# Kernel tuning notes

Hardware: AMD Instinct MI355X
Metric: run time of the kernel (lower is better)

The kernel has to match this reference:

```python
import jax, jax.numpy as jnp
import numpy as np

ATOM_DIM, HID, N_LAYERS, N_HEADS, PF_DIM = 34, 256, 2, 8, 1024
B, NA, NP = 32, 512, 1024


def setup_inputs() -> dict:
    key = jax.random.key(0)
    ks = iter(jax.random.split(key, 32))
    def rn(shape, s=0.02):
        return jax.random.normal(next(ks), shape, dtype=jnp.float32) * s
    L = N_LAYERS
    z = lambda *s: jnp.zeros(s, jnp.float32)
    return {
        "trg": jax.random.normal(next(ks), (B, NA, ATOM_DIM), dtype=jnp.float32),
        "src": jax.random.normal(next(ks), (B, NP, HID), dtype=jnp.float32),
        "ft_w": rn((HID, ATOM_DIM)), "ft_b": z(HID),
        "ln_g": jnp.ones((L, HID), jnp.float32), "ln_b": z(L, HID),
        "sa_wq": rn((L, HID, HID)), "sa_bq": z(L, HID),
        "sa_wk": rn((L, HID, HID)), "sa_bk": z(L, HID),
        "sa_wv": rn((L, HID, HID)), "sa_bv": z(L, HID),
        "sa_wf": rn((L, HID, HID)), "sa_bf": z(L, HID),
        "ea_wq": rn((L, HID, HID)), "ea_bq": z(L, HID),
        "ea_wk": rn((L, HID, HID)), "ea_bk": z(L, HID),
        "ea_wv": rn((L, HID, HID)), "ea_bv": z(L, HID),
        "ea_wf": rn((L, HID, HID)), "ea_bf": z(L, HID),
        "pf_w1": rn((L, PF_DIM, HID)), "pf_b1": z(L, PF_DIM),
        "pf_w2": rn((L, HID, PF_DIM)), "pf_b2": z(L, HID),
        "fc1_w": rn((256, HID)), "fc1_b": z(256),
        "fc2_w": rn((2, 256)), "fc2_b": z(2),
    }


def _ln(x, g, b, eps=1e-5):
    m = jnp.mean(x, axis=-1, keepdims=True)
    v = jnp.mean(jnp.square(x - m), axis=-1, keepdims=True)
    return (x - m) * jax.lax.rsqrt(v + eps) * g + b


def _attn(xq, xkv, wq, bq, wk, bk, wv, bv, wf, bf):
    b_, lq, h = xq.shape
    d = h // N_HEADS
    q = (xq @ wq.T + bq).reshape(b_, lq, N_HEADS, d).transpose(0, 2, 1, 3)
    k = (xkv @ wk.T + bk).reshape(b_, -1, N_HEADS, d).transpose(0, 2, 1, 3)
    v = (xkv @ wv.T + bv).reshape(b_, -1, N_HEADS, d).transpose(0, 2, 1, 3)
    scale = jnp.sqrt(jnp.float32(d))  # TransformerCPI: sqrt(hid_dim // n_heads)
    a = jax.nn.softmax(jnp.einsum('bhqd,bhkd->bhqk', q, k) / scale, axis=-1)
    o = jnp.einsum('bhqk,bhkd->bhqd', a, v).transpose(0, 2, 1, 3).reshape(b_, lq, h)
    return o @ wf.T + bf


def reference(trg, src, ft_w, ft_b, ln_g, ln_b,
              sa_wq, sa_bq, sa_wk, sa_bk, sa_wv, sa_bv, sa_wf, sa_bf,
              ea_wq, ea_bq, ea_wk, ea_bk, ea_wv, ea_bv, ea_wf, ea_bf,
              pf_w1, pf_b1, pf_w2, pf_b2, fc1_w, fc1_b, fc2_w, fc2_b):
    x = trg @ ft_w.T + ft_b  # [B, NA, HID]
    for l in range(N_LAYERS):
        x = _ln(x + _attn(x, x, sa_wq[l], sa_bq[l], sa_wk[l], sa_bk[l],
                          sa_wv[l], sa_bv[l], sa_wf[l], sa_bf[l]), ln_g[l], ln_b[l])
        x = _ln(x + _attn(x, src, ea_wq[l], ea_bq[l], ea_wk[l], ea_bk[l],
                          ea_wv[l], ea_bv[l], ea_wf[l], ea_bf[l]), ln_g[l], ln_b[l])
        h = jax.nn.relu(x @ pf_w1[l].T + pf_b1[l]) @ pf_w2[l].T + pf_b2[l]
        x = _ln(x + h, ln_g[l], ln_b[l])
    # norm-weighted attention pooling (replaces the nested Python loops)
    w = jax.nn.softmax(jnp.linalg.norm(x, axis=2), axis=1)  # [B, NA]
    pooled = jnp.einsum('bn,bnh->bh', w, x)  # [B, HID]
    return jax.nn.relu(pooled @ fc1_w.T + fc1_b) @ fc2_w.T + fc2_b
```

## Files before the change

kernel.cpp:

```cpp
#include <hip/hip_runtime.h>
#include <hip/hip_bf16.h>
#include <math.h>

#define B_   32
#define NA   512
#define NP   1024
#define HID  256
#define NH   8
#define DH   32
#define PF   1024

typedef short bf16x8 __attribute__((ext_vector_type(8)));
typedef float f32x4  __attribute__((ext_vector_type(4)));
typedef float f32x16 __attribute__((ext_vector_type(16)));
typedef unsigned u32x4 __attribute__((ext_vector_type(4)));

#define ZERO16 {0.f,0.f,0.f,0.f,0.f,0.f,0.f,0.f,0.f,0.f,0.f,0.f,0.f,0.f,0.f,0.f}

static __device__ inline unsigned short f2bf(float f) {
    __hip_bfloat16 h = __float2bfloat16(f);
    unsigned short u;
    __builtin_memcpy(&u, &h, 2);
    return u;
}
static __device__ inline float bf2f(unsigned short u) {
    unsigned x = ((unsigned)u) << 16;
    return __uint_as_float(x);
}
static __device__ inline unsigned cvtpk(float lo, float hi) {
    return (unsigned)f2bf(lo) | ((unsigned)f2bf(hi) << 16);
}
static __device__ inline bf16x8 pack8(float4 a, float4 b) {
    bf16x8 r;
    r[0] = (short)f2bf(a.x); r[1] = (short)f2bf(a.y);
    r[2] = (short)f2bf(a.z); r[3] = (short)f2bf(a.w);
    r[4] = (short)f2bf(b.x); r[5] = (short)f2bf(b.y);
    r[6] = (short)f2bf(b.z); r[7] = (short)f2bf(b.w);
    return r;
}
static __device__ inline void gload16(const unsigned short* g, unsigned short* l) {
    __builtin_amdgcn_global_load_lds(
        (const __attribute__((address_space(1))) void*)g,
        (__attribute__((address_space(3))) void*)l, 16, 0, 0);
}

__global__ __launch_bounds__(256) void ft_kernel(const float* __restrict__ trg,
    const float* __restrict__ w, const float* __restrict__ b,
    float* __restrict__ out, unsigned short* __restrict__ outb)
{
    __shared__ float Ws[256][35];
    int tid = threadIdx.x;
    for (int k = 0; k < 34; ++k) Ws[tid][k] = w[tid*34 + k];
    float bias = b[tid];
    __syncthreads();
    int m0 = blockIdx.x * 32;
    for (int r = 0; r < 32; ++r) {
        int m = m0 + r;
        const float* tr = trg + (size_t)m*34;
        float acc = bias;
        #pragma unroll
        for (int k = 0; k < 34; ++k) acc += tr[k] * Ws[tid][k];
        out [(size_t)m*HID + tid] = acc;
        outb[(size_t)m*HID + tid] = f2bf(acc);
    }
}

__global__ __launch_bounds__(256) void cvt_bf16(const float* __restrict__ in,
    unsigned short* __restrict__ outb, int n8)
{
    int i = blockIdx.x*256 + threadIdx.x;
    int stride = gridDim.x*256;
    for (; i < n8; i += stride) {
        float4 a = *(const float4*)(in + (size_t)i*8);
        float4 b = *(const float4*)(in + (size_t)i*8 + 4);
        *(bf16x8*)(outb + (size_t)i*8) = pack8(a, b);
    }
}

__global__ __launch_bounds__(256) void cvt_w(
    const float* __restrict__ s0, const float* __restrict__ s1,
    const float* __restrict__ s2, const float* __restrict__ s3,
    const float* __restrict__ s4, const float* __restrict__ s5,
    const float* __restrict__ s6, const float* __restrict__ s7,
    const float* __restrict__ s8, const float* __restrict__ s9,
    unsigned short* __restrict__ dst)
{
    const int z = blockIdx.z;
    const float* src;
    switch (z) {
        case 0: src = s0; break; case 1: src = s1; break;
        case 2: src = s2; break; case 3: src = s3; break;
        case 4: src = s4; break; case 5: src = s5; break;
        case 6: src = s6; break; case 7: src = s7; break;
        case 8: src = s8; break; default: src = s9; break;
    }
    const int n8 = (z < 8) ? 16384 : 65536;
    const size_t off = (z < 8) ? (size_t)z*131072 : (1048576u + (size_t)(z-8)*524288);
    unsigned short* o = dst + off;
    int i = blockIdx.x*256 + threadIdx.x;
    const int stride = gridDim.x*256;
    for (; i < n8; i += stride) {
        float4 a = *(const float4*)(src + (size_t)i*8);
        float4 b = *(const float4*)(src + (size_t)i*8 + 4);
        *(bf16x8*)(o + (size_t)i*8) = pack8(a, b);
    }
}

static __device__ inline void gemm_core(const unsigned short* __restrict__ Ab,
    const unsigned short* __restrict__ Wb, const float* __restrict__ bias,
    void* __restrict__ Cv, int M, int N, int K, int mode, int L, float oscale,
    int bx, int by)
{
    __shared__ __attribute__((aligned(16))) unsigned short As[2][128*64];
    __shared__ __attribute__((aligned(16))) unsigned short Ws[2][64*64];
    const int tid = threadIdx.x;
    const int wave = tid >> 6, lane = tid & 63, lq = lane & 15, g = lane >> 4;
    const int wr = wave >> 1, wc = wave & 1;
    const int m0 = by * 128, n0 = bx * 64;

    const int srow = lane >> 3;
    const int scol = ((lane & 7) ^ ((lane >> 3) & 7)) * 8;
    const int cswz = (lq & 7) * 8;

    f32x4 acc[4][2] = {};

    auto STAGE = [&](int kt, int buf) {
        const int k0 = kt * 64;
        #pragma unroll
        for (int c = 0; c < 4; ++c) {
            const int row = wave*32 + c*8;
            gload16(Ab + (size_t)(m0 + row + srow)*K + k0 + scol,
                    &As[buf][row*64]);
        }
        #pragma unroll
        for (int c = 0; c < 2; ++c) {
            const int row = wave*16 + c*8;
            gload16(Wb + (size_t)(n0 + row + srow)*K + k0 + scol,
                    &Ws[buf][row*64]);
        }
    };

    const int nk = K / 64;
    STAGE(0, 0);
    __syncthreads();
    for (int kt = 0; kt < nk; ++kt) {
        const int cur = kt & 1;
        if (kt + 1 < nk) STAGE(kt + 1, cur ^ 1);
        const unsigned short* Ac = &As[cur][0];
        const unsigned short* Wc = &Ws[cur][0];
        #pragma unroll
        for (int ks = 0; ks < 2; ++ks) {
            const int co = (ks*32 + g*8) ^ cswz;
            bf16x8 bf0 = *(const bf16x8*)&Wc[(wc*32 +  0 + lq)*64 + co];
            bf16x8 bf1 = *(const bf16x8*)&Wc[(wc*32 + 16 + lq)*64 + co];
            #pragma unroll
            for (int i = 0; i < 4; ++i) {
                bf16x8 af = *(const bf16x8*)&Ac[(wr*64 + i*16 + lq)*64 + co];
                acc[i][0] = __builtin_amdgcn_mfma_f32_16x16x32_bf16(af, bf0, acc[i][0], 0, 0, 0);
                acc[i][1] = __builtin_amdgcn_mfma_f32_16x16x32_bf16(af, bf1, acc[i][1], 0, 0, 0);
            }
        }
        __syncthreads();
    }

    float bb[2];
    #pragma unroll
    for (int j = 0; j < 2; ++j) bb[j] = bias[n0 + wc*32 + j*16 + lq];

    #pragma unroll
    for (int i = 0; i < 4; ++i) {
        const int mb = m0 + wr*64 + i*16 + 4*g;
        #pragma unroll
        for (int j = 0; j < 2; ++j) {
            const int n = n0 + wc*32 + j*16 + lq;
            f32x4 v = acc[i][j];
            #pragma unroll
            for (int r = 0; r < 4; ++r) v[r] = (v[r] + bb[j]) * oscale;
            if (mode == 1) {
                unsigned short* Cb = (unsigned short*)Cv;
                #pragma unroll
                for (int r = 0; r < 4; ++r) Cb[(size_t)(mb + r)*N + n] = f2bf(v[r]);
            } else if (mode == 3) {
                unsigned short* Cb = (unsigned short*)Cv;
                #pragma unroll
                for (int r = 0; r < 4; ++r) Cb[(size_t)(mb + r)*N + n] = f2bf(fmaxf(v[r], 0.f));
            } else if (mode == 4) {
                unsigned short* Cb = (unsigned short*)Cv;
                const int bI = mb / L, kk = mb % L;
                const int hh = n >> 5, d = n & 31;
                const int t2 = kk >> 5, dc = d >> 4, hi2 = (d >> 3) & 1;
                unsigned short* base = Cb
                    + ((size_t)(((bI*NH + hh)*(L >> 5) + t2)*2 + dc))*512
                    + ((kk & 31) + 32*hi2)*8 + (d & 7);
                base[0]  = f2bf(v[0]); base[8]  = f2bf(v[1]);
                base[16] = f2bf(v[2]); base[24] = f2bf(v[3]);
            } else {
                unsigned short* Cb = (unsigned short*)Cv;
                const int bI = mb / L, kk = mb % L;
                const int hh = n >> 5, d = n & 31;
                const int t = kk >> 6, oct = (kk >> 3) & 7;
                const int c = oct >> 1, hiV = oct & 1;
                ushort4 pk;
                pk.x = f2bf(v[0]); pk.y = f2bf(v[1]); pk.z = f2bf(v[2]); pk.w = f2bf(v[3]);
                *(ushort4*)(Cb
                    + ((size_t)(((bI*NH + hh)*(L >> 6) + t)*4 + c))*512
                    + (d + 32*hiV)*8 + (kk & 7)) = pk;
            }
        }
    }
}

static __device__ inline void xcd_swz(int d, int nx, int nxy, int& bx, int& by)
{
    const int w = (d & 7) * (nxy >> 3) + (d >> 3);
    bx = w % nx; by = w / nx;
}

__global__ __launch_bounds__(256) void gemm_mfma(const unsigned short* __restrict__ A,
    const unsigned short* __restrict__ W, const float* __restrict__ bias,
    void* __restrict__ C, int M, int N, int K, int mode, int L)
{
    int bx, by;
    xcd_swz(blockIdx.y*gridDim.x + blockIdx.x, gridDim.x, gridDim.x*gridDim.y, bx, by);
    gemm_core(A, W, bias, C, M, N, K, mode, L, 1.f, bx, by);
}

__global__ __launch_bounds__(256) void qkv_mfma(const unsigned short* __restrict__ Aq,
    const unsigned short* __restrict__ Akv,
    const unsigned short* __restrict__ Wq, const float* __restrict__ bq,
    const unsigned short* __restrict__ Wk, const float* __restrict__ bk,
    const unsigned short* __restrict__ Wv, const float* __restrict__ bv,
    void* __restrict__ qo, void* __restrict__ ko, void* __restrict__ vo,
    int Mq, int Mkv, int L)
{
    const int z = blockIdx.z;
    const unsigned short* A = (z == 0) ? Aq : Akv;
    const unsigned short* W = (z == 0) ? Wq : ((z == 1) ? Wk : Wv);
    const float* bb = (z == 0) ? bq : ((z == 1) ? bk : bv);
    void* C = (z == 0) ? qo : ((z == 1) ? ko : vo);
    const int M = (z == 0) ? Mq : Mkv;
    const int mode = (z == 0) ? 1 : ((z == 1) ? 4 : 5);
    const float sc = (z == 0) ? 0.25504082364238727f : 1.f;
    int bx, by;
    xcd_swz(blockIdx.y*gridDim.x + blockIdx.x, gridDim.x, gridDim.x*gridDim.y, bx, by);
    if (by * 128 >= M) return;
    gemm_core(A, W, bb, C, M, HID, HID, mode, L, sc, bx, by);
}

__global__ __launch_bounds__(512) void gemm_ln(const unsigned short* __restrict__ Ab,
    const unsigned short* __restrict__ Wb, const float* __restrict__ bias,
    const float* __restrict__ lng, const float* __restrict__ lnb,
    float* __restrict__ x, unsigned short* __restrict__ xb,
    float* __restrict__ nrm, int K)
{
    __shared__ __attribute__((aligned(16))) char smem[81920];
    unsigned short* As0 = (unsigned short*)smem;
    unsigned short* Ws0 = (unsigned short*)(smem + 16384);
    float* ys = (float*)smem;
    const int tid = threadIdx.x;
    const int w = tid >> 6, lane = tid & 63, lq = lane & 15, g = lane >> 4;
    const int wc2 = w & 3, wh = w >> 2;
    const int m0 = blockIdx.x * 64;

    const int srow = lane >> 3;
    const int scol = ((lane & 7) ^ srow) * 8;
    const int cswz = (lq & 7) * 8;

    f32x4 acc[4][2] = {};

    auto STAGE = [&](int kt, int buf) {
        const int k0 = kt * 64;
        {   const int row = w * 8;
            gload16(Ab + (size_t)(m0 + row + srow)*K + k0 + scol,
                    As0 + buf*4096 + row*64);
        }
        #pragma unroll
        for (int c = 0; c < 4; ++c) {
            const int row = w*32 + c*8;
            gload16(Wb + (size_t)(row + srow)*K + k0 + scol,
                    Ws0 + buf*16384 + row*64);
        }
    };

    const int nk = K / 64;
    STAGE(0, 0);
    __syncthreads();
    for (int kt = 0; kt < nk; ++kt) {
        const int cur = kt & 1;
        if (kt + 1 < nk) STAGE(kt + 1, cur ^ 1);
        const unsigned short* Ac = As0 + cur*4096;
        const unsigned short* Wc = Ws0 + cur*16384;
        #pragma unroll
        for (int ks = 0; ks < 2; ++ks) {
            const int co = (ks*32 + g*8) ^ cswz;
            bf16x8 bf0 = *(const bf16x8*)&Wc[(wc2*64 + wh*32 +  0 + lq)*64 + co];
            bf16x8 bf1 = *(const bf16x8*)&Wc[(wc2*64 + wh*32 + 16 + lq)*64 + co];
            #pragma unroll
            for (int i = 0; i < 4; ++i) {
                bf16x8 af = *(const bf16x8*)&Ac[(i*16 + lq)*64 + co];
                acc[i][0] = __builtin_amdgcn_mfma_f32_16x16x32_bf16(af, bf0, acc[i][0], 0, 0, 0);
                acc[i][1] = __builtin_amdgcn_mfma_f32_16x16x32_bf16(af, bf1, acc[i][1], 0, 0, 0);
            }
        }
        __syncthreads();
    }

    float bb0 = bias[wc2*64 + wh*32 +  0 + lq];
    float bb1 = bias[wc2*64 + wh*32 + 16 + lq];
    #pragma unroll
    for (int i = 0; i < 4; ++i) {
        const int col0 = wc2*64 + wh*32 + lq;
        #pragma unroll
        for (int r = 0; r < 4; ++r) {
            const int row = i*16 + 4*g + r;
            ys[row*260 + col0]      = acc[i][0][r] + bb0;
            ys[row*260 + col0 + 16] = acc[i][1][r] + bb1;
        }
    }
    __syncthreads();

    float4 gv = *(const float4*)(lng + lane*4);
    float4 bv = *(const float4*)(lnb + lane*4);
    for (int it = 0; it < 8; ++it) {
        const int row = w*8 + it;
        const size_t gbase = (size_t)(m0 + row)*HID + lane*4;
        float4 y = *(float4*)&ys[row*260 + lane*4];
        float4 xv = *(const float4*)(x + gbase);
        y.x += xv.x; y.y += xv.y; y.z += xv.z; y.w += xv.w;
        float s = y.x + y.y + y.z + y.w;
        #pragma unroll
        for (int o = 32; o > 0; o >>= 1) s += __shfl_xor(s, o);
        float mean = s * (1.f/256.f);
        float4 d = {y.x - mean, y.y - mean, y.z - mean, y.w - mean};
        float q2 = d.x*d.x + d.y*d.y + d.z*d.z + d.w*d.w;
        #pragma unroll
        for (int o = 32; o > 0; o >>= 1) q2 += __shfl_xor(q2, o);
        float rs = rsqrtf(q2*(1.f/256.f) + 1e-5f);
        float4 ov;
        ov.x = d.x*rs*gv.x + bv.x; ov.y = d.y*rs*gv.y + bv.y;
        ov.z = d.z*rs*gv.z + bv.z; ov.w = d.w*rs*gv.w + bv.w;
        *(float4*)(x + gbase) = ov;
        ushort4 pk;
        pk.x = f2bf(ov.x); pk.y = f2bf(ov.y); pk.z = f2bf(ov.z); pk.w = f2bf(ov.w);
        *(ushort4*)(xb + gbase) = pk;
        if (nrm) {
            float q3 = ov.x*ov.x + ov.y*ov.y + ov.z*ov.z + ov.w*ov.w;
            #pragma unroll
            for (int o = 32; o > 0; o >>= 1) q3 += __shfl_xor(q3, o);
            if (lane == 0) nrm[m0 + row] = sqrtf(q3);
        }
    }
}

__global__ __launch_bounds__(256) void attn_mfma(const unsigned short* __restrict__ Qb,
    const unsigned short* __restrict__ KF, const unsigned short* __restrict__ VF,
    unsigned short* __restrict__ O, int Lk)
{
    __shared__ float Ll[4][32];
    const int orig = blockIdx.x;
    const int sw = (orig & 7) * 128 + (orig >> 3);
    const int qt = sw & 3;
    const int h  = (sw >> 2) & 7;
    const int b  = sw >> 5;
    const int tid = threadIdx.x, w = tid >> 6, lane = tid & 63;
    const int q32 = lane & 31, hi = lane >> 5;

    const unsigned short* qp = Qb + ((size_t)(b*NA + qt*128 + w*32 + q32))*HID + h*DH + hi*8;
    bf16x8 qf0 = *(const bf16x8*)qp;
    bf16x8 qf1 = *(const bf16x8*)(qp + 16);

    const unsigned short* Kf = KF + (size_t)((b*NH + h)*(Lk >> 5)*2)*512 + lane*8;
    const unsigned short* Vf = VF + (size_t)((b*NH + h)*(Lk >> 6)*4)*512 + lane*8;

    f32x16 o_acc = ZERO16;
    float lacc = 0.f;

    bf16x8 kfA[4], kfB[4], vfT[4];
    auto LOADK = [&](int t, bf16x8* kd) {
        #pragma unroll
        for (int f = 0; f < 4; ++f)
            kd[f] = *(const bf16x8*)(Kf + (size_t)(t*4 + f)*512);
    };
    auto STEP = [&](const bf16x8* kf, int t) {
        #pragma unroll
        for (int c = 0; c < 4; ++c)
            vfT[c] = *(const bf16x8*)(Vf + (size_t)(t*4 + c)*512);
        f32x16 st0 = ZERO16, st1 = ZERO16;
        st0 = __builtin_amdgcn_mfma_f32_32x32x16_bf16(kf[0], qf0, st0, 0, 0, 0);
        st0 = __builtin_amdgcn_mfma_f32_32x32x16_bf16(kf[1], qf1, st0, 0, 0, 0);
        st1 = __builtin_amdgcn_mfma_f32_32x32x16_bf16(kf[2], qf0, st1, 0, 0, 0);
        st1 = __builtin_amdgcn_mfma_f32_32x32x16_bf16(kf[3], qf1, st1, 0, 0, 0);
        bf16x8 pa[4];
        float lp = 0.f;
        #pragma unroll
        for (int c = 0; c < 4; ++c) {
            const f32x16& s = (c < 2) ? st0 : st1;
            const int rb = (c & 1) * 8;
            float p0 = __builtin_amdgcn_exp2f(s[rb+0]);
            float p1 = __builtin_amdgcn_exp2f(s[rb+1]);
            float p2 = __builtin_amdgcn_exp2f(s[rb+2]);
            float p3 = __builtin_amdgcn_exp2f(s[rb+3]);
            float p4 = __builtin_amdgcn_exp2f(s[rb+4]);
            float p5 = __builtin_amdgcn_exp2f(s[rb+5]);
            float p6 = __builtin_amdgcn_exp2f(s[rb+6]);
            float p7 = __builtin_amdgcn_exp2f(s[rb+7]);
            lp += (p0+p1) + (p2+p3) + (p4+p5) + (p6+p7);
            unsigned A1 = cvtpk(p0, p1), A2 = cvtpk(p2, p3);
            unsigned B1 = cvtpk(p4, p5), B2 = cvtpk(p6, p7);
            auto r1 = __builtin_amdgcn_permlane32_swap(A1, B1, false, false);
            auto r2 = __builtin_amdgcn_permlane32_swap(A2, B2, false, false);
            u32x4 pw; pw[0] = r1[0]; pw[1] = r2[0]; pw[2] = r1[1]; pw[3] = r2[1];
            __builtin_memcpy(&pa[c], &pw, 16);
        }
        lacc += lp;
        #pragma unroll
        for (int c = 0; c < 4; ++c)
            o_acc = __builtin_amdgcn_mfma_f32_32x32x16_bf16(pa[c], vfT[c], o_acc, 0, 0, 0);
    };

    const int nt = Lk >> 6;
    LOADK(0, kfA);
    for (int t = 0; t < nt; t += 2) {
        LOADK(t + 1, kfB);
        STEP(kfA, t);
        if (t + 2 < nt) LOADK(t + 2, kfA);
        STEP(kfB, t + 1);
    }

    float lt = lacc + __shfl_xor(lacc, 32);
    float linv = 1.f / lt;
    if (hi == 0) Ll[w][q32] = linv;
    f32x4 li[4];
    #pragma unroll
    for (int jg = 0; jg < 4; ++jg) li[jg] = *(const f32x4*)&Ll[w][jg*8 + hi*4];

    unsigned short* Op = O + ((size_t)(b*NA + qt*128 + w*32))*HID + h*DH + q32;
    #pragma unroll
    for (int jg = 0; jg < 4; ++jg) {
        #pragma unroll
        for (int r2 = 0; r2 < 4; ++r2) {
            const int q = jg*8 + hi*4 + r2;
            Op[(size_t)q*HID] = f2bf(o_acc[jg*4 + r2] * li[jg][r2]);
        }
    }
}

__global__ __launch_bounds__(256) void pooled_k(const float* __restrict__ x,
    const float* __restrict__ nw, float* __restrict__ pooled)
{
    __shared__ float sw[NA];
    __shared__ float red[256];
    __shared__ float part[8][33];
    const int b = blockIdx.x, hc = blockIdx.y;
    const int tid = threadIdx.x;
    const float* nb = nw + (size_t)b*NA;
    float v0 = nb[tid], v1 = nb[tid + 256];
    red[tid] = fmaxf(v0, v1); __syncthreads();
    for (int s = 128; s > 0; s >>= 1) { if (tid < s) red[tid] = fmaxf(red[tid], red[tid+s]); __syncthreads(); }
    float mx = red[0]; __syncthreads();
    float e0 = __expf(v0 - mx), e1 = __expf(v1 - mx);
    sw[tid] = e0; sw[tid + 256] = e1;
    red[tid] = e0 + e1; __syncthreads();
    for (int s = 128; s > 0; s >>= 1) { if (tid < s) red[tid] += red[tid+s]; __syncthreads(); }
    float inv = 1.f / red[0];
    __syncthreads();
    const int ng = tid >> 5, col = tid & 31;
    const float* xp = x + (size_t)b*NA*HID + hc*32 + col;
    float acc = 0.f;
    for (int n = ng; n < NA; n += 8)
        acc += sw[n] * xp[(size_t)n*HID];
    part[ng][col] = acc;
    __syncthreads();
    if (tid < 32) {
        float s = 0.f;
        #pragma unroll
        for (int i = 0; i < 8; ++i) s += part[i][tid];
        pooled[(size_t)b*HID + hc*32 + tid] = s * inv;
    }
}

__global__ __launch_bounds__(256) void head_k(const float* __restrict__ pooled,
    const float* __restrict__ fc1w, const float* __restrict__ fc1b,
    const float* __restrict__ fc2w, const float* __restrict__ fc2b,
    float* __restrict__ out)
{
    __shared__ float p[HID];
    __shared__ float a1[HID];
    const int b = blockIdx.x, tid = threadIdx.x;
    p[tid] = pooled[(size_t)b*HID + tid];
    __syncthreads();
    float s1 = fc1b[tid];
    const float* w1 = fc1w + (size_t)tid*HID;
    for (int k2 = 0; k2 < HID; k2 += 4) {
        float4 w = *(const float4*)(w1 + k2);
        s1 += p[k2]*w.x + p[k2+1]*w.y + p[k2+2]*w.z + p[k2+3]*w.w;
    }
    a1[tid] = fmaxf(s1, 0.f);
    __syncthreads();
    if (tid < 2) {
        float s2 = fc2b[tid];
        const float* w2 = fc2w + (size_t)tid*HID;
        for (int k2 = 0; k2 < HID; ++k2) s2 += a1[k2] * w2[k2];
        out[b*2 + tid] = s2;
    }
}

extern "C" void kernel_launch(void* const* d_in, const int* in_sizes, int n_in,
                              void* d_out, int out_size, void* d_ws, size_t ws_size,
                              hipStream_t stream)
{
    const float* trg  = (const float*)d_in[0];
    const float* src  = (const float*)d_in[1];
    const float* ft_w = (const float*)d_in[2];
    const float* ft_b = (const float*)d_in[3];
    const float* ln_g = (const float*)d_in[4];
    const float* ln_b = (const float*)d_in[5];
    const float* sa_wq = (const float*)d_in[6];  const float* sa_bq = (const float*)d_in[7];
    const float* sa_wk = (const float*)d_in[8];  const float* sa_bk = (const float*)d_in[9];
    const float* sa_wv = (const float*)d_in[10]; const float* sa_bv = (const float*)d_in[11];
    const float* sa_wf = (const float*)d_in[12]; const float* sa_bf = (const float*)d_in[13];
    const float* ea_wq = (const float*)d_in[14]; const float* ea_bq = (const float*)d_in[15];
    const float* ea_wk = (const float*)d_in[16]; const float* ea_bk = (const float*)d_in[17];
    const float* ea_wv = (const float*)d_in[18]; const float* ea_bv = (const float*)d_in[19];
    const float* ea_wf = (const float*)d_in[20]; const float* ea_bf = (const float*)d_in[21];
    const float* pf_w1 = (const float*)d_in[22]; const float* pf_b1 = (const float*)d_in[23];
    const float* pf_w2 = (const float*)d_in[24]; const float* pf_b2 = (const float*)d_in[25];
    const float* fc1w  = (const float*)d_in[26]; const float* fc1b  = (const float*)d_in[27];
    const float* fc2w  = (const float*)d_in[28]; const float* fc2b  = (const float*)d_in[29];
    float* out = (float*)d_out;

    const size_t NTOK = (size_t)B_*NA;
    const size_t NSRC = (size_t)B_*NP;
    float* ws = (float*)d_ws;
    float* x  = ws;
    float* nw = x + NTOK*HID;
    float* pooled = nw + NTOK;
    unsigned short* xb   = (unsigned short*)(pooled + B_*HID);
    unsigned short* tb   = xb + NTOK*HID;
    unsigned short* srcb = tb + NTOK*HID;
    unsigned short* qb   = srcb + NSRC*HID;
    unsigned short* kb   = qb + NTOK*HID;
    unsigned short* vTb  = kb + NSRC*HID;
    unsigned short* wb   = vTb + NSRC*HID;
    unsigned short* hb   = qb;

    unsigned short* saq_b = wb;
    unsigned short* sak_b = wb +  131072;
    unsigned short* sav_b = wb +  262144;
    unsigned short* saf_b = wb +  393216;
    unsigned short* eaq_b = wb +  524288;
    unsigned short* eak_b = wb +  655360;
    unsigned short* eav_b = wb +  786432;
    unsigned short* eaf_b = wb +  917504;
    unsigned short* pw1_b = wb + 1048576;
    unsigned short* pw2_b = wb + 1572864;

    const int M = (int)NTOK;
    dim3 blk(256);

    cvt_w<<<dim3(64, 1, 10), blk, 0, stream>>>(sa_wq, sa_wk, sa_wv, sa_wf,
        ea_wq, ea_wk, ea_wv, ea_wf, pf_w1, pf_w2, wb);
    ft_kernel<<<M/32, blk, 0, stream>>>(trg, ft_w, ft_b, x, xb);
    cvt_bf16<<<1024, blk, 0, stream>>>(src, srcb, (int)(NSRC*HID/8));

    for (int l = 0; l < 2; ++l) {
        const size_t wo = (size_t)l*HID*HID, bo = (size_t)l*HID;
        qkv_mfma<<<dim3(HID/64, M/128, 3), blk, 0, stream>>>(xb, xb,
            saq_b+wo, sa_bq+bo, sak_b+wo, sa_bk+bo, sav_b+wo, sa_bv+bo,
            qb, kb, vTb, M, M, NA);
        attn_mfma<<<dim3(1024), blk, 0, stream>>>(qb, kb, vTb, tb, NA);
        gemm_ln<<<dim3(M/64), dim3(512), 0, stream>>>(tb, saf_b+wo, sa_bf+bo,
            ln_g+bo, ln_b+bo, x, xb, nullptr, HID);
        qkv_mfma<<<dim3(HID/64, (int)NSRC/128, 3), blk, 0, stream>>>(xb, srcb,
            eaq_b+wo, ea_bq+bo, eak_b+wo, ea_bk+bo, eav_b+wo, ea_bv+bo,
            qb, kb, vTb, M, (int)NSRC, NP);
        attn_mfma<<<dim3(1024), blk, 0, stream>>>(qb, kb, vTb, tb, NP);
        gemm_ln<<<dim3(M/64), dim3(512), 0, stream>>>(tb, eaf_b+wo, ea_bf+bo,
            ln_g+bo, ln_b+bo, x, xb, nullptr, HID);
        gemm_mfma<<<dim3(PF/64, M/128), blk, 0, stream>>>(xb, pw1_b+(size_t)l*PF*HID, pf_b1+(size_t)l*PF, hb, M, PF, HID, 3, 0);
        gemm_ln<<<dim3(M/64), dim3(512), 0, stream>>>(hb, pw2_b+(size_t)l*HID*PF, pf_b2+bo,
            ln_g+bo, ln_b+bo, x, xb, (l == 1) ? nw : nullptr, PF);
    }

    pooled_k<<<dim3(B_, 8), blk, 0, stream>>>(x, nw, pooled);
    head_k<<<B_, blk, 0, stream>>>(pooled, fc1w, fc1b, fc2w, fc2b, out);
}
```

Measured before the change: 417.3 us.

## Widen GEMM tile to 128x128 and drop LDS double buffering

The shared GEMM core moves from a 128x64 to a 128x128 output tile, so each wave computes a 64x64 sub-tile with 16 accumulators and reuses every A fragment four times. LDS double buffering is removed: each k-step now loads, syncs, and computes synchronously, keeping LDS use at 32KB. Launch grids for the QKV and FFN1 GEMMs are halved in N to match. The aim is more MFMA work per LDS read and fewer blocks, at the cost of losing load/compute overlap and cutting the block count, which may hurt occupancy for these small GEMMs.

```diff
diff --git a/kernel.cpp b/kernel.cpp
--- a/kernel.cpp
+++ b/kernel.cpp
@@ -111,68 +111,61 @@
     void* __restrict__ Cv, int M, int N, int K, int mode, int L, float oscale,
     int bx, int by)
 {
-    __shared__ __attribute__((aligned(16))) unsigned short As[2][128*64];
-    __shared__ __attribute__((aligned(16))) unsigned short Ws[2][64*64];
+    __shared__ __attribute__((aligned(16))) unsigned short As[128*64];
+    __shared__ __attribute__((aligned(16))) unsigned short Bs[128*64];
     const int tid = threadIdx.x;
     const int wave = tid >> 6, lane = tid & 63, lq = lane & 15, g = lane >> 4;
     const int wr = wave >> 1, wc = wave & 1;
-    const int m0 = by * 128, n0 = bx * 64;
+    const int m0 = by * 128, n0 = bx * 128;
 
     const int srow = lane >> 3;
-    const int scol = ((lane & 7) ^ ((lane >> 3) & 7)) * 8;
+    const int scol = ((lane & 7) ^ srow) * 8;
     const int cswz = (lq & 7) * 8;
 
-    f32x4 acc[4][2] = {};
-
-    auto STAGE = [&](int kt, int buf) {
+    f32x4 acc[4][4] = {};
+
+    auto STAGE = [&](int kt) {
         const int k0 = kt * 64;
         #pragma unroll
         for (int c = 0; c < 4; ++c) {
             const int row = wave*32 + c*8;
-            gload16(Ab + (size_t)(m0 + row + srow)*K + k0 + scol,
-                    &As[buf][row*64]);
-        }
-        #pragma unroll
-        for (int c = 0; c < 2; ++c) {
-            const int row = wave*16 + c*8;
-            gload16(Wb + (size_t)(n0 + row + srow)*K + k0 + scol,
-                    &Ws[buf][row*64]);
+            gload16(Ab + (size_t)(m0 + row + srow)*K + k0 + scol, &As[row*64]);
+            gload16(Wb + (size_t)(n0 + row + srow)*K + k0 + scol, &Bs[row*64]);
         }
     };
 
     const int nk = K / 64;
-    STAGE(0, 0);
-    __syncthreads();
     for (int kt = 0; kt < nk; ++kt) {
-        const int cur = kt & 1;
-        if (kt + 1 < nk) STAGE(kt + 1, cur ^ 1);
-        const unsigned short* Ac = &As[cur][0];
-        const unsigned short* Wc = &Ws[cur][0];
+        __syncthreads();
+        STAGE(kt);
+        __syncthreads();
         #pragma unroll
         for (int ks = 0; ks < 2; ++ks) {
             const int co = (ks*32 + g*8) ^ cswz;
-            bf16x8 bf0 = *(const bf16x8*)&Wc[(wc*32 +  0 + lq)*64 + co];
-            bf16x8 bf1 = *(const bf16x8*)&Wc[(wc*32 + 16 + lq)*64 + co];
+            bf16x8 bfr[4];
+            #pragma unroll
+            for (int j = 0; j < 4; ++j)
+                bfr[j] = *(const bf16x8*)&Bs[(wc*64 + j*16 + lq)*64 + co];
             #pragma unroll
             for (int i = 0; i < 4; ++i) {
-                bf16x8 af = *(const bf16x8*)&Ac[(wr*64 + i*16 + lq)*64 + co];
-                acc[i][0] = __builtin_amdgcn_mfma_f32_16x16x32_bf16(af, bf0, acc[i][0], 0, 0, 0);
-                acc[i][1] = __builtin_amdgcn_mfma_f32_16x16x32_bf16(af, bf1, acc[i][1], 0, 0, 0);
+                bf16x8 af = *(const bf16x8*)&As[(wr*64 + i*16 + lq)*64 + co];
+                #pragma unroll
+                for (int j = 0; j < 4; ++j)
+                    acc[i][j] = __builtin_amdgcn_mfma_f32_16x16x32_bf16(af, bfr[j], acc[i][j], 0, 0, 0);
             }
         }
-        __syncthreads();
-    }
-
-    float bb[2];
+    }
+
+    float bb[4];
     #pragma unroll
-    for (int j = 0; j < 2; ++j) bb[j] = bias[n0 + wc*32 + j*16 + lq];
+    for (int j = 0; j < 4; ++j) bb[j] = bias[n0 + wc*64 + j*16 + lq];
 
     #pragma unroll
     for (int i = 0; i < 4; ++i) {
         const int mb = m0 + wr*64 + i*16 + 4*g;
         #pragma unroll
-        for (int j = 0; j < 2; ++j) {
-            const int n = n0 + wc*32 + j*16 + lq;
+        for (int j = 0; j < 4; ++j) {
+            const int n = n0 + wc*64 + j*16 + lq;
             f32x4 v = acc[i][j];
             #pragma unroll
             for (int r = 0; r < 4; ++r) v[r] = (v[r] + bb[j]) * oscale;
@@ -565,19 +558,19 @@
 
     for (int l = 0; l < 2; ++l) {
         const size_t wo = (size_t)l*HID*HID, bo = (size_t)l*HID;
-        qkv_mfma<<<dim3(HID/64, M/128, 3), blk, 0, stream>>>(xb, xb,
+        qkv_mfma<<<dim3(HID/128, M/128, 3), blk, 0, stream>>>(xb, xb,
             saq_b+wo, sa_bq+bo, sak_b+wo, sa_bk+bo, sav_b+wo, sa_bv+bo,
             qb, kb, vTb, M, M, NA);
         attn_mfma<<<dim3(1024), blk, 0, stream>>>(qb, kb, vTb, tb, NA);
         gemm_ln<<<dim3(M/64), dim3(512), 0, stream>>>(tb, saf_b+wo, sa_bf+bo,
             ln_g+bo, ln_b+bo, x, xb, nullptr, HID);
-        qkv_mfma<<<dim3(HID/64, (int)NSRC/128, 3), blk, 0, stream>>>(xb, srcb,
+        qkv_mfma<<<dim3(HID/128, (int)NSRC/128, 3), blk, 0, stream>>>(xb, srcb,
             eaq_b+wo, ea_bq+bo, eak_b+wo, ea_bk+bo, eav_b+wo, ea_bv+bo,
             qb, kb, vTb, M, (int)NSRC, NP);
         attn_mfma<<<dim3(1024), blk, 0, stream>>>(qb, kb, vTb, tb, NP);
         gemm_ln<<<dim3(M/64), dim3(512), 0, stream>>>(tb, eaf_b+wo, ea_bf+bo,
             ln_g+bo, ln_b+bo, x, xb, nullptr, HID);
-        gemm_mfma<<<dim3(PF/64, M/128), blk, 0, stream>>>(xb, pw1_b+(size_t)l*PF*HID, pf_b1+(size_t)l*PF, hb, M, PF, HID, 3, 0);
+        gemm_mfma<<<dim3(PF/128, M/128), blk, 0, stream>>>(xb, pw1_b+(size_t)l*PF*HID, pf_b1+(size_t)l*PF, hb, M, PF, HID, 3, 0);
         gemm_ln<<<dim3(M/64), dim3(512), 0, stream>>>(hb, pw2_b+(size_t)l*HID*PF, pf_b2+bo,
             ln_g+bo, ln_b+bo, x, xb, (l == 1) ? nw : nullptr, PF);
     }
```

New measurement: 522.1 us. 1.25x slower.
